# Kernel tuning notes

Measured on AMD Instinct MI355X. Metric: run time of the kernel, lower is better.

The kernel has to match this reference:

```python
import jax, jax.numpy as jnp
import numpy as np

B, L, D_MODEL, D_INNER, P = 4, 16384, 256, 512, 64  # P = d_state, conj_sym=False
STEP_RESCALE = 1.0


def setup_inputs() -> dict:
    key = jax.random.key(0)
    ks = jax.random.split(key, 11)
    # projections (bias=False)
    W_in = jax.random.normal(ks[0], (D_MODEL, 2 * D_INNER), jnp.float32) * (1.0 / np.sqrt(D_MODEL))
    W_out = jax.random.normal(ks[1], (D_INNER, D_MODEL), jnp.float32) * (1.0 / np.sqrt(D_INNER))
    # diagonal SSM params: Lambda = A_real + i*A_imag, HiPPO-like (negative real part)
    A_real = -0.5 * jnp.ones((P,), jnp.float32) - jax.random.uniform(ks[2], (P,), jnp.float32)
    A_imag = jnp.pi * jnp.arange(P, dtype=jnp.float32) * (jax.random.uniform(ks[3], (P,), jnp.float32) * 0.1 + 0.95)
    B_re = jax.random.normal(ks[4], (P, D_INNER), jnp.float32) * (1.0 / np.sqrt(P))
    B_im = jax.random.normal(ks[5], (P, D_INNER), jnp.float32) * (1.0 / np.sqrt(P))
    C_re = jax.random.normal(ks[6], (D_INNER, P), jnp.float32) * (1.0 / np.sqrt(D_INNER))
    C_im = jax.random.normal(ks[7], (D_INNER, P), jnp.float32) * (1.0 / np.sqrt(D_INNER))
    D = jax.random.normal(ks[8], (D_INNER,), jnp.float32)
    # dt ~ loguniform[dt_min, dt_max]; inv_dt = softplus^{-1}(dt) = dt + log(-expm1(-dt))
    dt = jnp.exp(jax.random.uniform(ks[9], (P,), jnp.float32) * (np.log(0.1) - np.log(0.001)) + np.log(0.001))
    dt = jnp.clip(dt, 1e-4, None)
    inv_dt = dt + jnp.log(-jnp.expm1(-dt))
    x = jax.random.normal(ks[10], (B, L, D_MODEL), jnp.float32)
    return {"x": x, "W_in": W_in, "W_out": W_out, "A_real": A_real, "A_imag": A_imag,
            "B_re": B_re, "B_im": B_im, "C_re": C_re, "C_im": C_im, "D": D, "inv_dt": inv_dt}


def _binop(e1, e2):
    a1, b1 = e1
    a2, b2 = e2
    return a2 * a1, a2 * b1 + b2


def reference(x, W_in, W_out, A_real, A_imag, B_re, B_im, C_re, C_im, D, inv_dt):
    # in_proj + gate split
    x_and_res = x @ W_in                       # (b, l, 2*d_inner)
    u, res = jnp.split(x_and_res, 2, axis=-1)
    u = jax.nn.silu(u)                         # (b, l, d_inner)
    # bilinear discretization of diagonal SSM
    A = A_real + 1j * A_imag                   # (P,)
    dt = STEP_RESCALE * jax.nn.softplus(inv_dt)  # (P,)
    BL = 1.0 / (1.0 - (dt / 2.0) * A)
    dA = BL * (1.0 + (dt / 2.0) * A)           # (P,)
    dB = (BL * dt)[:, None] * (B_re + 1j * B_im)  # (P, d_inner)
    # drive: Bu_t = dB @ u_t
    Bu = u.astype(dA.dtype) @ dB.T             # (b, l, P) complex
    # parallel (associative) scan of h_t = dA*h_{t-1} + Bu_t  (h_0 = 0)
    elems = (jnp.broadcast_to(dA, Bu.shape), Bu)
    _, h = jax.lax.associative_scan(_binop, elems, axis=1)  # (b, l, P)
    C = C_re + 1j * C_im                       # (d_inner, P)
    y = jnp.real(h @ C.T) + D * u              # (b, l, d_inner), + skip D*u
    y = y * jax.nn.silu(res)
    return y @ W_out                           # (b, l, d_model)
```

## Files before the change

### kernel.cpp

```cpp
#include <hip/hip_runtime.h>
#include <math.h>

#define NTOK 65536
#define LSEQ 16384
#define GCH 64
#define NCH 256

typedef __attribute__((ext_vector_type(8))) short short8v;
typedef __attribute__((ext_vector_type(4))) float f32x4;
typedef unsigned short u16;

__device__ __forceinline__ u16 f2bf(float f) {
  unsigned u = __float_as_uint(f);
  return (u16)((u + 0x7FFFu + ((u >> 16) & 1u)) >> 16);
}
__device__ __forceinline__ float bf2f(u16 b) {
  return __uint_as_float(((unsigned)b) << 16);
}
__device__ __forceinline__ unsigned cvtpk_bf16(float lo, float hi) {
  unsigned r;
  asm("v_cvt_pk_bf16_f32 %0, %1, %2" : "=v"(r) : "v"(lo), "v"(hi));
  return r;
}
__device__ __forceinline__ float silu_f(float v) {
  return v * __builtin_amdgcn_rcpf(1.f + __expf(-v));
}
__device__ __forceinline__ void gld16(const u16* g, u16* l) {
  __builtin_amdgcn_global_load_lds((const __attribute__((address_space(1))) void*)g,
                                   (__attribute__((address_space(3))) void*)l, 16, 0, 0);
}

#define WAITV4 asm volatile("s_waitcnt vmcnt(4) lgkmcnt(0)" ::: "memory")
#define WAITV0 asm volatile("s_waitcnt vmcnt(0) lgkmcnt(0)" ::: "memory")
#define BARRAW asm volatile("s_barrier" ::: "memory")

__global__ void setup_scalar_k(const float* __restrict__ A_real, const float* __restrict__ A_imag,
                               const float* __restrict__ inv_dt,
                               float2* __restrict__ dAf, float2* __restrict__ fvec,
                               float2* __restrict__ powt) {
  int p = threadIdx.x;
  if (p >= 64) return;
  double ar = (double)A_real[p], ai = (double)A_imag[p];
  double dt = log1p(exp((double)inv_dt[p]));
  double zr = 0.5 * dt * ar, zi = 0.5 * dt * ai;
  double d1r = 1.0 - zr;
  double den = d1r * d1r + zi * zi;
  double blr = d1r / den, bli = zi / den;
  double nr = 1.0 + zr, ni = zi;
  double dar = blr * nr - bli * ni;
  double dai = blr * ni + bli * nr;
  dAf[p] = make_float2((float)dar, (float)dai);
  fvec[p] = make_float2((float)(blr * dt), (float)(bli * dt));
  double cr = 1.0, ci = 0.0;
  for (int k = 0; k <= GCH; ++k) {
    powt[p * (GCH + 1) + k] = make_float2((float)cr, (float)ci);
    double t = cr * dar - ci * dai;
    ci = cr * dai + ci * dar;
    cr = t;
  }
}

__global__ void setup_tables_k(const float* __restrict__ B_re, const float* __restrict__ B_im,
                               const float* __restrict__ C_re, const float* __restrict__ C_im,
                               const float* __restrict__ W_in, const float* __restrict__ W_out,
                               const float2* __restrict__ fvec,
                               u16* __restrict__ WinT, u16* __restrict__ dBn,
                               u16* __restrict__ Ccb, u16* __restrict__ WoutT) {
  int idx = blockIdx.x * blockDim.x + threadIdx.x;
  int stride = gridDim.x * blockDim.x;
  for (int i = idx; i < 1024 * 256; i += stride) {
    int n = i >> 8, k = i & 255;
    WinT[i] = f2bf(W_in[k * 1024 + n]);
  }
  for (int i = idx; i < 128 * 512; i += stride) {
    int p = i >> 9, d = i & 511;
    float2 f = fvec[p & 63];
    float br = B_re[(p & 63) * 512 + d], bi = B_im[(p & 63) * 512 + d];
    float v = (p < 64) ? (f.x * br - f.y * bi) : (f.x * bi + f.y * br);
    dBn[i] = f2bf(v);
  }
  for (int i = idx; i < 512 * 128; i += stride) {
    int d = i >> 7, k = i & 127;
    float v = (k < 64) ? C_re[d * 64 + k] : -C_im[d * 64 + (k - 64)];
    Ccb[i] = f2bf(v);
  }
  for (int i = idx; i < 256 * 512; i += stride) {
    int n = i >> 9, k = i & 511;
    WoutT[i] = f2bf(W_out[k * 256 + n]);
  }
}

__global__ __launch_bounds__(256) void cvt_x_k(const float* __restrict__ x, u16* __restrict__ xb) {
  size_t i = ((size_t)blockIdx.x * blockDim.x + threadIdx.x) * 4;
  size_t stride = (size_t)gridDim.x * blockDim.x * 4;
  const size_t total = (size_t)NTOK * 256;
  for (; i < total; i += stride) {
    float4 v = *(const float4*)(x + i);
    ushort4 o;
    o.x = f2bf(v.x); o.y = f2bf(v.y); o.z = f2bf(v.z); o.w = f2bf(v.w);
    *(ushort4*)(xb + i) = o;
  }
}

template<int MODE, int LOG_NBX, int KDIM>
__global__ __launch_bounds__(256) void mgemm(
    const u16* __restrict__ A, const u16* __restrict__ Bt,
    void* __restrict__ C0, void* __restrict__ C1,
    const float* __restrict__ Dvec) {
  __shared__ u16 As[3][128 * 32];
  __shared__ u16 Bs[3][128 * 32];
  const int tid = threadIdx.x;
  const int w = tid >> 6, l = tid & 63;
  const int wm = w >> 1, wn = w & 1;

  const int lin = blockIdx.x;
  const int cpx = gridDim.x >> 3;
  const int swz = (lin & 7) * cpx + (lin >> 3);
  const int n0 = (swz & ((1 << LOG_NBX) - 1)) * 128;
  const int m0 = (swz >> LOG_NBX) * 128;

  f32x4 acc[4][4] = {};

  const int lr = l >> 2;
  const int sc = (l & 3) ^ ((l >> 3) & 3);
  const u16* gA = A + (size_t)(m0 + w * 32 + lr) * KDIM + sc * 8;
  const u16* gB = Bt + (size_t)(n0 + w * 32 + lr) * KDIM + sc * 8;
  const size_t rowskip = (size_t)16 * KDIM;

  const int fr = l & 15;
  const int kgs = (((l >> 4) ^ (l >> 1)) & 3) * 8;

  constexpr int NT = KDIM / 32;

  auto stage = [&](int buf, int k0) {
    u16* lA = &As[buf][w * 1024];
    u16* lB = &Bs[buf][w * 1024];
    gld16(gA + k0, lA);
    gld16(gA + k0 + rowskip, lA + 512);
    gld16(gB + k0, lB);
    gld16(gB + k0 + rowskip, lB + 512);
  };
  auto compute = [&](int buf) {
    short8v af[4], bfr[4];
#pragma unroll
    for (int mi = 0; mi < 4; ++mi)
      af[mi] = *(const short8v*)&As[buf][(wm * 64 + mi * 16 + fr) * 32 + kgs];
#pragma unroll
    for (int ni = 0; ni < 4; ++ni)
      bfr[ni] = *(const short8v*)&Bs[buf][(wn * 64 + ni * 16 + fr) * 32 + kgs];
#pragma unroll
    for (int mi = 0; mi < 4; ++mi)
#pragma unroll
      for (int ni = 0; ni < 4; ++ni)
        acc[mi][ni] = __builtin_amdgcn_mfma_f32_16x16x32_bf16(af[mi], bfr[ni], acc[mi][ni], 0, 0, 0);
  };

  stage(0, 0);
  if (NT > 1) stage(1, 32);
#pragma unroll
  for (int t = 0; t < NT; ++t) {
    if (t + 1 < NT) { WAITV4; } else { WAITV0; }
    BARRAW;
    if (t + 2 < NT) stage((t + 2) % 3, (t + 2) * 32);
    compute(t % 3);
  }

  const int rbase = (l >> 4) * 4;
#pragma unroll
  for (int mi = 0; mi < 4; ++mi) {
#pragma unroll
    for (int ni = 0; ni < 4; ++ni) {
      int gr0 = m0 + wm * 64 + mi * 16 + rbase;
      int gc = n0 + wn * 64 + ni * 16 + fr;
      if (MODE == 0) {
        float s0 = silu_f(acc[mi][ni][0]);
        float s1 = silu_f(acc[mi][ni][1]);
        float s2 = silu_f(acc[mi][ni][2]);
        float s3 = silu_f(acc[mi][ni][3]);
        unsigned p01 = cvtpk_bf16(s0, s1);
        unsigned p23 = cvtpk_bf16(s2, s3);
        u16* Cw = (n0 < 512) ? (u16*)C0 : (u16*)C1;
        int col = gc - ((n0 < 512) ? 0 : 512);
        Cw[(size_t)(gr0 + 0) * 512 + col] = (u16)p01;
        Cw[(size_t)(gr0 + 1) * 512 + col] = (u16)(p01 >> 16);
        Cw[(size_t)(gr0 + 2) * 512 + col] = (u16)p23;
        Cw[(size_t)(gr0 + 3) * 512 + col] = (u16)(p23 >> 16);
      } else if (MODE == 1) {
#pragma unroll
        for (int j = 0; j < 4; ++j)
          ((float*)C0)[(size_t)(gr0 + j) * 128 + gc] = acc[mi][ni][j];
      } else if (MODE == 2) {
        float g[4];
#pragma unroll
        for (int j = 0; j < 4; ++j) {
          size_t r = (size_t)(gr0 + j);
          float uu = bf2f(((const u16*)C0)[r * 512 + gc]);
          float sr = bf2f(((const u16*)C1)[r * 512 + gc]);
          g[j] = (acc[mi][ni][j] + Dvec[gc] * uu) * sr;
        }
        unsigned p01 = cvtpk_bf16(g[0], g[1]);
        unsigned p23 = cvtpk_bf16(g[2], g[3]);
        ((u16*)C1)[(size_t)(gr0 + 0) * 512 + gc] = (u16)p01;
        ((u16*)C1)[(size_t)(gr0 + 1) * 512 + gc] = (u16)(p01 >> 16);
        ((u16*)C1)[(size_t)(gr0 + 2) * 512 + gc] = (u16)p23;
        ((u16*)C1)[(size_t)(gr0 + 3) * 512 + gc] = (u16)(p23 >> 16);
      } else {
#pragma unroll
        for (int j = 0; j < 4; ++j)
          ((float*)C0)[(size_t)(gr0 + j) * 256 + gc] = acc[mi][ni][j];
      }
    }
  }
}

__global__ __launch_bounds__(256) void scan_local_k(float* __restrict__ Bu, const float2* __restrict__ dAf) {
  int unit = blockIdx.x * 4 + (threadIdx.x >> 6);
  int p = threadIdx.x & 63;
  int b = unit >> 8, c = unit & 255;
  float2 dA = dAf[p];
  size_t base = ((size_t)b * LSEQ + (size_t)c * GCH) * 128;
  float hr = 0.f, hi = 0.f;
  for (int i0 = 0; i0 < GCH; i0 += 8) {
    float br[8], bi[8];
#pragma unroll
    for (int j = 0; j < 8; ++j) {
      br[j] = Bu[base + (size_t)(i0 + j) * 128 + p];
      bi[j] = Bu[base + (size_t)(i0 + j) * 128 + 64 + p];
    }
#pragma unroll
    for (int j = 0; j < 8; ++j) {
      float nr = fmaf(dA.x, hr, fmaf(-dA.y, hi, br[j]));
      float ni = fmaf(dA.x, hi, fmaf(dA.y, hr, bi[j]));
      hr = nr; hi = ni; br[j] = hr; bi[j] = hi;
    }
#pragma unroll
    for (int j = 0; j < 8; ++j) {
      Bu[base + (size_t)(i0 + j) * 128 + p] = br[j];
      Bu[base + (size_t)(i0 + j) * 128 + 64 + p] = bi[j];
    }
  }
}

__global__ void scan_carry_k(const float* __restrict__ Bu, float* __restrict__ offc,
                             const float2* __restrict__ powt) {
  int b = threadIdx.x >> 6;
  int p = threadIdx.x & 63;
  float2 dAG = powt[p * (GCH + 1) + GCH];
  float rr = 0.f, ri = 0.f;
  for (int c0 = 0; c0 < NCH; c0 += 8) {
    float er[8], ei[8];
#pragma unroll
    for (int j = 0; j < 8; ++j) {
      size_t n = (size_t)b * LSEQ + (size_t)(c0 + j) * GCH + (GCH - 1);
      er[j] = Bu[n * 128 + p];
      ei[j] = Bu[n * 128 + 64 + p];
    }
#pragma unroll
    for (int j = 0; j < 8; ++j) {
      size_t orow = (size_t)(b * NCH + c0 + j) * 128;
      offc[orow + p] = rr;
      offc[orow + 64 + p] = ri;
      float nr = fmaf(dAG.x, rr, fmaf(-dAG.y, ri, er[j]));
      float ni = fmaf(dAG.x, ri, fmaf(dAG.y, rr, ei[j]));
      rr = nr; ri = ni;
    }
  }
}

__global__ __launch_bounds__(256) void fixup_k(const float* __restrict__ Bu, const float* __restrict__ offc,
                                               const float2* __restrict__ powt, u16* __restrict__ hb) {
  size_t idx = (size_t)blockIdx.x * blockDim.x + threadIdx.x;
  const size_t total = (size_t)NTOK * 64;
  size_t stride = (size_t)gridDim.x * blockDim.x;
  for (; idx < total; idx += stride) {
    int p = (int)(idx & 63);
    size_t n = idx >> 6;
    int l = (int)(n & (LSEQ - 1));
    int i = l & (GCH - 1);
    float2 pw = powt[p * (GCH + 1) + i + 1];
    size_t crow = (n >> 6) * 128;
    float orr = offc[crow + p], oii = offc[crow + 64 + p];
    float hr = Bu[n * 128 + p]      + pw.x * orr - pw.y * oii;
    float hi = Bu[n * 128 + 64 + p] + pw.x * oii + pw.y * orr;
    hb[n * 128 + p] = f2bf(hr);
    hb[n * 128 + 64 + p] = f2bf(hi);
  }
}

extern "C" void kernel_launch(void* const* d_in, const int* in_sizes, int n_in,
                              void* d_out, int out_size, void* d_ws, size_t ws_size,
                              hipStream_t stream) {
  const float* x      = (const float*)d_in[0];
  const float* W_in   = (const float*)d_in[1];
  const float* W_out  = (const float*)d_in[2];
  const float* A_real = (const float*)d_in[3];
  const float* A_imag = (const float*)d_in[4];
  const float* B_re   = (const float*)d_in[5];
  const float* B_im   = (const float*)d_in[6];
  const float* C_re   = (const float*)d_in[7];
  const float* C_im   = (const float*)d_in[8];
  const float* Dv     = (const float*)d_in[9];
  const float* inv_dt = (const float*)d_in[10];

  u16* xb    = (u16*)d_ws;
  u16* u_bf  = xb + (size_t)NTOK * 256;
  u16* sr_bf = u_bf + (size_t)NTOK * 512;
  u16* h_bf  = sr_bf + (size_t)NTOK * 512;
  u16* WinT  = h_bf + (size_t)NTOK * 128;
  u16* dBn   = WinT + 1024 * 256;
  u16* Ccb   = dBn + 128 * 512;
  u16* WoutT = Ccb + 512 * 128;

  float* O    = (float*)d_out;
  float* Bu   = O;
  float* offc = O + 8388608;
  float2* powt = (float2*)(O + 8519680);
  float2* dAf  = (float2*)(O + 8528000);
  float2* fvec = (float2*)(O + 8528128);

  setup_scalar_k<<<1, 64, 0, stream>>>(A_real, A_imag, inv_dt, dAf, fvec, powt);
  setup_tables_k<<<256, 256, 0, stream>>>(B_re, B_im, C_re, C_im, W_in, W_out, fvec,
                                          WinT, dBn, Ccb, WoutT);
  cvt_x_k<<<1024, 256, 0, stream>>>(x, xb);

  mgemm<0, 3, 256><<<4096, 256, 0, stream>>>(xb, WinT, u_bf, sr_bf, nullptr);
  mgemm<1, 0, 512><<<512, 256, 0, stream>>>(u_bf, dBn, Bu, nullptr, nullptr);
  scan_local_k<<<256, 256, 0, stream>>>(Bu, dAf);
  scan_carry_k<<<1, 256, 0, stream>>>(Bu, offc, powt);
  fixup_k<<<4096, 256, 0, stream>>>(Bu, offc, powt, h_bf);
  mgemm<2, 2, 128><<<2048, 256, 0, stream>>>(h_bf, Ccb, u_bf, sr_bf, Dv);
  mgemm<3, 1, 512><<<1024, 256, 0, stream>>>(sr_bf, WoutT, O, nullptr, nullptr);
}
```

Measured before the change: 237.3 us.

## Use 8-wave GEMM tiles and restructure scan into sum/carry/emit passes

The GEMM kernel now runs 512 threads per block with an 2x4 wave grid, each wave computing a 64x32 sub-tile and issuing one async LDS load per operand per stage, with the wait count adjusted to match. The chunked scan no longer writes local prefix states back to Bu. A first pass computes only each chunk's final state into a small carry buffer. The emit pass rescans each chunk starting from its carried-in offset and writes bf16 h directly, replacing the power-table fixup kernel and one full fp32 write/read of Bu. The trade-offs are fewer accumulators but more waves per block in the GEMM, and a serial rescan in place of the elementwise fixup.

After: 210.2 us. 1.13x faster.

```diff
diff --git a/kernel.cpp b/kernel.cpp
--- a/kernel.cpp
+++ b/kernel.cpp
@@ -30,7 +30,7 @@
                                    (__attribute__((address_space(3))) void*)l, 16, 0, 0);
 }
 
-#define WAITV4 asm volatile("s_waitcnt vmcnt(4) lgkmcnt(0)" ::: "memory")
+#define WAITV2 asm volatile("s_waitcnt vmcnt(2) lgkmcnt(0)" ::: "memory")
 #define WAITV0 asm volatile("s_waitcnt vmcnt(0) lgkmcnt(0)" ::: "memory")
 #define BARRAW asm volatile("s_barrier" ::: "memory")
 
@@ -103,7 +103,7 @@
 }
 
 template<int MODE, int LOG_NBX, int KDIM>
-__global__ __launch_bounds__(256) void mgemm(
+__global__ __launch_bounds__(512) void mgemm(
     const u16* __restrict__ A, const u16* __restrict__ Bt,
     void* __restrict__ C0, void* __restrict__ C1,
     const float* __restrict__ Dvec) {
@@ -111,7 +111,7 @@
   __shared__ u16 Bs[3][128 * 32];
   const int tid = threadIdx.x;
   const int w = tid >> 6, l = tid & 63;
-  const int wm = w >> 1, wn = w & 1;
+  const int wm = w >> 2, wn = w & 3;
 
   const int lin = blockIdx.x;
   const int cpx = gridDim.x >> 3;
@@ -119,13 +119,12 @@
   const int n0 = (swz & ((1 << LOG_NBX) - 1)) * 128;
   const int m0 = (swz >> LOG_NBX) * 128;
 
-  f32x4 acc[4][4] = {};
+  f32x4 acc[4][2] = {};
 
   const int lr = l >> 2;
   const int sc = (l & 3) ^ ((l >> 3) & 3);
-  const u16* gA = A + (size_t)(m0 + w * 32 + lr) * KDIM + sc * 8;
-  const u16* gB = Bt + (size_t)(n0 + w * 32 + lr) * KDIM + sc * 8;
-  const size_t rowskip = (size_t)16 * KDIM;
+  const u16* gA = A + (size_t)(m0 + w * 16 + lr) * KDIM + sc * 8;
+  const u16* gB = Bt + (size_t)(n0 + w * 16 + lr) * KDIM + sc * 8;
 
   const int fr = l & 15;
   const int kgs = (((l >> 4) ^ (l >> 1)) & 3) * 8;
@@ -133,25 +132,21 @@
   constexpr int NT = KDIM / 32;
 
   auto stage = [&](int buf, int k0) {
-    u16* lA = &As[buf][w * 1024];
-    u16* lB = &Bs[buf][w * 1024];
-    gld16(gA + k0, lA);
-    gld16(gA + k0 + rowskip, lA + 512);
-    gld16(gB + k0, lB);
-    gld16(gB + k0 + rowskip, lB + 512);
+    gld16(gA + k0, &As[buf][w * 512]);
+    gld16(gB + k0, &Bs[buf][w * 512]);
   };
   auto compute = [&](int buf) {
-    short8v af[4], bfr[4];
+    short8v af[4], bfr[2];
 #pragma unroll
     for (int mi = 0; mi < 4; ++mi)
       af[mi] = *(const short8v*)&As[buf][(wm * 64 + mi * 16 + fr) * 32 + kgs];
 #pragma unroll
-    for (int ni = 0; ni < 4; ++ni)
-      bfr[ni] = *(const short8v*)&Bs[buf][(wn * 64 + ni * 16 + fr) * 32 + kgs];
+    for (int ni = 0; ni < 2; ++ni)
+      bfr[ni] = *(const short8v*)&Bs[buf][(wn * 32 + ni * 16 + fr) * 32 + kgs];
 #pragma unroll
     for (int mi = 0; mi < 4; ++mi)
 #pragma unroll
-      for (int ni = 0; ni < 4; ++ni)
+      for (int ni = 0; ni < 2; ++ni)
         acc[mi][ni] = __builtin_amdgcn_mfma_f32_16x16x32_bf16(af[mi], bfr[ni], acc[mi][ni], 0, 0, 0);
   };
 
@@ -159,7 +154,7 @@
   if (NT > 1) stage(1, 32);
 #pragma unroll
   for (int t = 0; t < NT; ++t) {
-    if (t + 1 < NT) { WAITV4; } else { WAITV0; }
+    if (t + 1 < NT) { WAITV2; } else { WAITV0; }
     BARRAW;
     if (t + 2 < NT) stage((t + 2) % 3, (t + 2) * 32);
     compute(t % 3);
@@ -169,9 +164,9 @@
 #pragma unroll
   for (int mi = 0; mi < 4; ++mi) {
 #pragma unroll
-    for (int ni = 0; ni < 4; ++ni) {
+    for (int ni = 0; ni < 2; ++ni) {
       int gr0 = m0 + wm * 64 + mi * 16 + rbase;
-      int gc = n0 + wn * 64 + ni * 16 + fr;
+      int gc = n0 + wn * 32 + ni * 16 + fr;
       if (MODE == 0) {
         float s0 = silu_f(acc[mi][ni][0]);
         float s1 = silu_f(acc[mi][ni][1]);
@@ -213,13 +208,15 @@
   }
 }
 
-__global__ __launch_bounds__(256) void scan_local_k(float* __restrict__ Bu, const float2* __restrict__ dAf) {
+__global__ __launch_bounds__(256) void scan_sum_k(const float* __restrict__ Bu,
+                                                  float* __restrict__ carr,
+                                                  const float2* __restrict__ dAf) {
   int unit = blockIdx.x * 4 + (threadIdx.x >> 6);
   int p = threadIdx.x & 63;
   int b = unit >> 8, c = unit & 255;
   float2 dA = dAf[p];
   size_t base = ((size_t)b * LSEQ + (size_t)c * GCH) * 128;
-  float hr = 0.f, hi = 0.f;
+  float rr = 0.f, ri = 0.f;
   for (int i0 = 0; i0 < GCH; i0 += 8) {
     float br[8], bi[8];
 #pragma unroll
@@ -229,19 +226,16 @@
     }
 #pragma unroll
     for (int j = 0; j < 8; ++j) {
-      float nr = fmaf(dA.x, hr, fmaf(-dA.y, hi, br[j]));
-      float ni = fmaf(dA.x, hi, fmaf(dA.y, hr, bi[j]));
-      hr = nr; hi = ni; br[j] = hr; bi[j] = hi;
-    }
-#pragma unroll
-    for (int j = 0; j < 8; ++j) {
-      Bu[base + (size_t)(i0 + j) * 128 + p] = br[j];
-      Bu[base + (size_t)(i0 + j) * 128 + 64 + p] = bi[j];
-    }
-  }
-}
-
-__global__ void scan_carry_k(const float* __restrict__ Bu, float* __restrict__ offc,
+      float nr = fmaf(dA.x, rr, fmaf(-dA.y, ri, br[j]));
+      float ni = fmaf(dA.x, ri, fmaf(dA.y, rr, bi[j]));
+      rr = nr; ri = ni;
+    }
+  }
+  carr[(size_t)unit * 128 + p] = rr;
+  carr[(size_t)unit * 128 + 64 + p] = ri;
+}
+
+__global__ void scan_carry_k(const float* __restrict__ carr, float* __restrict__ offc,
                              const float2* __restrict__ powt) {
   int b = threadIdx.x >> 6;
   int p = threadIdx.x & 63;
@@ -251,9 +245,9 @@
     float er[8], ei[8];
 #pragma unroll
     for (int j = 0; j < 8; ++j) {
-      size_t n = (size_t)b * LSEQ + (size_t)(c0 + j) * GCH + (GCH - 1);
-      er[j] = Bu[n * 128 + p];
-      ei[j] = Bu[n * 128 + 64 + p];
+      size_t crow = (size_t)(b * NCH + c0 + j) * 128;
+      er[j] = carr[crow + p];
+      ei[j] = carr[crow + 64 + p];
     }
 #pragma unroll
     for (int j = 0; j < 8; ++j) {
@@ -267,23 +261,32 @@
   }
 }
 
-__global__ __launch_bounds__(256) void fixup_k(const float* __restrict__ Bu, const float* __restrict__ offc,
-                                               const float2* __restrict__ powt, u16* __restrict__ hb) {
-  size_t idx = (size_t)blockIdx.x * blockDim.x + threadIdx.x;
-  const size_t total = (size_t)NTOK * 64;
-  size_t stride = (size_t)gridDim.x * blockDim.x;
-  for (; idx < total; idx += stride) {
-    int p = (int)(idx & 63);
-    size_t n = idx >> 6;
-    int l = (int)(n & (LSEQ - 1));
-    int i = l & (GCH - 1);
-    float2 pw = powt[p * (GCH + 1) + i + 1];
-    size_t crow = (n >> 6) * 128;
-    float orr = offc[crow + p], oii = offc[crow + 64 + p];
-    float hr = Bu[n * 128 + p]      + pw.x * orr - pw.y * oii;
-    float hi = Bu[n * 128 + 64 + p] + pw.x * oii + pw.y * orr;
-    hb[n * 128 + p] = f2bf(hr);
-    hb[n * 128 + 64 + p] = f2bf(hi);
+__global__ __launch_bounds__(256) void scan_emit_k(const float* __restrict__ Bu,
+                                                   const float* __restrict__ offc,
+                                                   u16* __restrict__ hb,
+                                                   const float2* __restrict__ dAf) {
+  int unit = blockIdx.x * 4 + (threadIdx.x >> 6);
+  int p = threadIdx.x & 63;
+  int b = unit >> 8, c = unit & 255;
+  float2 dA = dAf[p];
+  size_t base = ((size_t)b * LSEQ + (size_t)c * GCH) * 128;
+  float hr = offc[(size_t)unit * 128 + p];
+  float hi = offc[(size_t)unit * 128 + 64 + p];
+  for (int i0 = 0; i0 < GCH; i0 += 8) {
+    float br[8], bi[8];
+#pragma unroll
+    for (int j = 0; j < 8; ++j) {
+      br[j] = Bu[base + (size_t)(i0 + j) * 128 + p];
+      bi[j] = Bu[base + (size_t)(i0 + j) * 128 + 64 + p];
+    }
+#pragma unroll
+    for (int j = 0; j < 8; ++j) {
+      float nr = fmaf(dA.x, hr, fmaf(-dA.y, hi, br[j]));
+      float ni = fmaf(dA.x, hi, fmaf(dA.y, hr, bi[j]));
+      hr = nr; hi = ni;
+      hb[base + (size_t)(i0 + j) * 128 + p] = f2bf(hr);
+      hb[base + (size_t)(i0 + j) * 128 + 64 + p] = f2bf(hi);
+    }
   }
 }
 
@@ -314,20 +317,21 @@
   float* O    = (float*)d_out;
   float* Bu   = O;
   float* offc = O + 8388608;
-  float2* powt = (float2*)(O + 8519680);
-  float2* dAf  = (float2*)(O + 8528000);
-  float2* fvec = (float2*)(O + 8528128);
+  float* carr = O + 8519680;
+  float2* powt = (float2*)(O + 8650752);
+  float2* dAf  = (float2*)(O + 8659072);
+  float2* fvec = (float2*)(O + 8659200);
 
   setup_scalar_k<<<1, 64, 0, stream>>>(A_real, A_imag, inv_dt, dAf, fvec, powt);
   setup_tables_k<<<256, 256, 0, stream>>>(B_re, B_im, C_re, C_im, W_in, W_out, fvec,
                                           WinT, dBn, Ccb, WoutT);
   cvt_x_k<<<1024, 256, 0, stream>>>(x, xb);
 
-  mgemm<0, 3, 256><<<4096, 256, 0, stream>>>(xb, WinT, u_bf, sr_bf, nullptr);
-  mgemm<1, 0, 512><<<512, 256, 0, stream>>>(u_bf, dBn, Bu, nullptr, nullptr);
-  scan_local_k<<<256, 256, 0, stream>>>(Bu, dAf);
-  scan_carry_k<<<1, 256, 0, stream>>>(Bu, offc, powt);
-  fixup_k<<<4096, 256, 0, stream>>>(Bu, offc, powt, h_bf);
-  mgemm<2, 2, 128><<<2048, 256, 0, stream>>>(h_bf, Ccb, u_bf, sr_bf, Dv);
-  mgemm<3, 1, 512><<<1024, 256, 0, stream>>>(sr_bf, WoutT, O, nullptr, nullptr);
-}
+  mgemm<0, 3, 256><<<4096, 512, 0, stream>>>(xb, WinT, u_bf, sr_bf, nullptr);
+  mgemm<1, 0, 512><<<512, 512, 0, stream>>>(u_bf, dBn, Bu, nullptr, nullptr);
+  scan_sum_k<<<256, 256, 0, stream>>>(Bu, carr, dAf);
+  scan_carry_k<<<1, 256, 0, stream>>>(carr, offc, powt);
+  scan_emit_k<<<256, 256, 0, stream>>>(Bu, offc, h_bf, dAf);
+  mgemm<2, 2, 128><<<2048, 512, 0, stream>>>(h_bf, Ccb, u_bf, sr_bf, Dv);
+  mgemm<3, 1, 512><<<1024, 512, 0, stream>>>(sr_bf, WoutT, O, nullptr, nullptr);
+}
```
